# Kernel optimization log

Hardware: AMD Instinct MI355X
Metric: run time of the kernel (lower is better)

## Reference

```python
import math
import jax, jax.numpy as jnp
import numpy as np

I_DIM = 64
N_MODES = 16
FACTOR = 4
EPS = 1e-5


def group_norm(x, w, b):
    # x: [B, M, N, C] channels-last; torch GroupNorm(C//16, C) over (group_channels, M, N)
    B, M, N, C = x.shape
    g = C // 16
    xr = x.reshape(B, M, N, g, C // g)
    mean = xr.mean(axis=(1, 2, 4), keepdims=True)
    var = xr.var(axis=(1, 2, 4), keepdims=True)
    xr = (xr - mean) * jax.lax.rsqrt(var + EPS)
    return xr.reshape(B, M, N, C) * w + b


def feed_forward(x, res, l1w, l1b, l2w, l2b, g1w, g1b, g2w, g2b, g3w, g3b):
    h = x @ l1w + l1b                      # [B,M,N,C*factor]
    h = group_norm(h, g1w, g1b)            # fork_1
    h = jax.nn.relu(h)
    h = h @ l2w + l2b                      # [B,M,N,C]
    h = group_norm(h, g2w, g2b)            # fork_2
    h = res + h
    h = group_norm(h, g3w, g3b)            # fork_3
    return h


def setup_inputs() -> dict:
    key = jax.random.key(0)
    ks = jax.random.split(key, 20)
    B, M, N, I = 4, 128, 128, I_DIM
    H = I * FACTOR
    z = jax.random.normal(ks[0], (B, 2 * M * N * I, 1), dtype=jnp.float32)
    x = jax.random.normal(ks[1], (B, M * N * I, 1), dtype=jnp.float32)
    # fourier weights [in, out, nm, nm, 2], xavier-ish scale
    fw_scale = math.sqrt(2.0 / (I + I))
    fw1 = jax.random.normal(ks[2], (I, I, N_MODES, N_MODES, 2), dtype=jnp.float32) * fw_scale
    fw2 = jax.random.normal(ks[3], (I, I, N_MODES, N_MODES, 2), dtype=jnp.float32) * fw_scale
    def ff_params(k0):
        kk = jax.random.split(k0, 4)
        return dict(
            l1w=jax.random.normal(kk[0], (I, H), dtype=jnp.float32) * math.sqrt(2.0 / (I + H)),
            l1b=jnp.zeros((H,), jnp.float32),
            l2w=jax.random.normal(kk[1], (H, I), dtype=jnp.float32) * math.sqrt(2.0 / (I + H)),
            l2b=jnp.zeros((I,), jnp.float32),
            g1w=jnp.ones((H,), jnp.float32), g1b=jnp.zeros((H,), jnp.float32),
            g2w=jnp.ones((I,), jnp.float32), g2b=jnp.zeros((I,), jnp.float32),
            g3w=jnp.ones((I,), jnp.float32), g3b=jnp.zeros((I,), jnp.float32),
        )
    bp = ff_params(ks[4])
    fp = ff_params(ks[5])
    out = {"z": z, "x": x, "fw1": fw1, "fw2": fw2}
    for name, p in (("b", bp), ("f", fp)):
        for k, v in p.items():
            out[f"{name}_{k}"] = v
    return out


def reference(z, x, fw1, fw2,
              b_l1w, b_l1b, b_l2w, b_l2b, b_g1w, b_g1b, b_g2w, b_g2b, b_g3w, b_g3b,
              f_l1w, f_l1b, f_l2w, f_l2b, f_g1w, f_g1b, f_g2w, f_g2b, f_g3w, f_g3b):
    I = I_DIM
    nm = N_MODES
    B = x.shape[0]
    M = N = int(math.sqrt(x.shape[1] // I))
    x4 = x.reshape(B, M, N, I)
    z5 = z.reshape(B, 2, M, N, I)
    backcast, forecast = z5[:, 0], z5[:, 1]
    x4 = x4 - backcast
    xc = jnp.transpose(x4, (0, 3, 1, 2))          # [B, I, M, N]
    x_ft = jnp.fft.rfft2(xc, s=(M, N), norm='ortho')  # [B, I, M, N//2+1] complex64
    w1 = fw1[..., 0] + 1j * fw1[..., 1]
    w2 = fw2[..., 0] + 1j * fw2[..., 1]
    top = jnp.einsum('bixy,ioxy->boxy', x_ft[:, :, :nm, :nm], w1)
    bot = jnp.einsum('bixy,ioxy->boxy', x_ft[:, :, -nm:, :nm], w2)
    out_ft = jnp.zeros((B, I, N, M // 2 + 1), dtype=x_ft.dtype)
    out_ft = out_ft.at[:, :, :nm, :nm].set(top).at[:, :, -nm:, :nm].set(bot)
    xo = jnp.fft.irfft2(out_ft, s=(N, M), norm='ortho')  # [B, I, M, N]
    xo = jnp.transpose(xo, (0, 2, 3, 1))                  # [B, M, N, I]
    backcast = feed_forward(xo, backcast, b_l1w, b_l1b, b_l2w, b_l2b,
                            b_g1w, b_g1b, b_g2w, b_g2b, b_g3w, b_g3b)
    forecast = feed_forward(xo, forecast, f_l1w, f_l1b, f_l2w, f_l2b,
                            f_g1w, f_g1b, f_g2w, f_g2b, f_g3w, f_g3b)
    out = jnp.stack([backcast, forecast], axis=1)         # [B, 2, M, N, I]
    return out.reshape(B, 2 * M * N * I, 1)
```

## Files before the change

kernel.cpp:

```cpp
#include <hip/hip_runtime.h>
#include <hip/hip_bf16.h>

typedef __hip_bfloat16 bf16;
typedef __attribute__((ext_vector_type(8))) short short8;
typedef __attribute__((ext_vector_type(4))) float f32x4;

#define PI2 6.283185307179586f
#define EPSV 1e-5f

__device__ __forceinline__ short f2bs(float f){
  bf16 h = __float2bfloat16(f);
  short s; __builtin_memcpy(&s, &h, 2); return s;
}
__device__ __forceinline__ float s2f(short s){
  bf16 h; __builtin_memcpy(&h, &s, 2); return __bfloat162float(h);
}
__device__ __forceinline__ float4 f4add(float4 a, float4 b){ return make_float4(a.x+b.x, a.y+b.y, a.z+b.z, a.w+b.w); }
__device__ __forceinline__ float4 f4sub(float4 a, float4 b){ return make_float4(a.x-b.x, a.y-b.y, a.z-b.z, a.w-b.w); }

__global__ __launch_bounds__(256) void k_prep_ydft(
    const float* __restrict__ x, const float* __restrict__ z,
    const float* __restrict__ fw1, const float* __restrict__ fw2,
    float2* __restrict__ FWT,
    const float* __restrict__ b_l1w, const float* __restrict__ b_l1b,
    const float* __restrict__ b_l2w, const float* __restrict__ b_l2b,
    const float* __restrict__ b_g1w, const float* __restrict__ b_g1b,
    const float* __restrict__ b_g2w, const float* __restrict__ b_g2b,
    const float* __restrict__ b_g3w, const float* __restrict__ b_g3b,
    const float* __restrict__ f_l1w, const float* __restrict__ f_l1b,
    const float* __restrict__ f_l2w, const float* __restrict__ f_l2b,
    const float* __restrict__ f_g1w, const float* __restrict__ f_g1b,
    const float* __restrict__ f_g2w, const float* __restrict__ f_g2b,
    const float* __restrict__ f_g3w, const float* __restrict__ f_g3b,
    short* __restrict__ W1g, short* __restrict__ W2g,
    float2* __restrict__ TWY, float2* __restrict__ TWX,
    float* __restrict__ PB, float* __restrict__ ST,
    float2* __restrict__ Y){
  __shared__ __align__(16) char sm[36864];
  int tid = threadIdx.x;
  int bi = blockIdx.x;
  if(bi < 512){
    float2 (*PQ)[64] = (float2(*)[64])sm;
    float2 (*RS)[64] = (float2(*)[64])(sm + 16384);
    float4 (*twl)[32] = (float4(*)[32])(sm + 32768);
    int b = bi >> 7, m = bi & 127;
    const float4* xp = (const float4*)(x + ((size_t)(b*128 + m)*128)*64);
    const float4* zp = (const float4*)(z + ((size_t)((b*2 + 0)*128 + m)*128)*64);
    int i4 = tid & 15, n0 = tid >> 4;
    #pragma unroll
    for(int it = 0; it < 2; it++){
      int np = n0 + it*16;
      float4 ea = f4sub(xp[np*16 + i4],      zp[np*16 + i4]);
      float4 eb = f4sub(xp[(np+32)*16 + i4], zp[(np+32)*16 + i4]);
      float4 ec = f4sub(xp[(np+64)*16 + i4], zp[(np+64)*16 + i4]);
      float4 ed = f4sub(xp[(np+96)*16 + i4], zp[(np+96)*16 + i4]);
      float4 sac = f4add(ea, ec), sbd = f4add(eb, ed);
      float4 P = f4add(sac, sbd), Q = f4sub(sac, sbd);
      float4 R = f4sub(ea, ec),  S = f4sub(eb, ed);
      *(float4*)&PQ[np][i4*4]     = make_float4(P.x, Q.x, P.y, Q.y);
      *(float4*)&PQ[np][i4*4 + 2] = make_float4(P.z, Q.z, P.w, Q.w);
      *(float4*)&RS[np][i4*4]     = make_float4(R.x, S.x, R.y, S.y);
      *(float4*)&RS[np][i4*4 + 2] = make_float4(R.z, S.z, R.w, S.w);
    }
    {
      int kq2 = tid >> 5, np = tid & 31;
      int ky0 = (kq2 >> 1)*4 + (kq2 & 1)*2;
      float s0, c0, s1, c1;
      sincosf(PI2*(float)((ky0*np) & 127)/128.f, &s0, &c0);
      sincosf(PI2*(float)(((ky0+1)*np) & 127)/128.f, &s1, &c1);
      twl[kq2][np] = make_float4(c0, s0, c1, s1);
    }
    __syncthreads();
    int i = tid & 63, kq = tid >> 6;
    float re[4] = {0,0,0,0}, im[4] = {0,0,0,0};
    for(int np = 0; np < 32; np++){
      float2 pq = PQ[np][i];
      float2 rs = RS[np][i];
      float4 t01 = twl[kq*2][np];
      float4 t23 = twl[kq*2 + 1][np];
      re[0] += pq.x*t01.x;               im[0] -= pq.x*t01.y;
      re[1] += rs.x*t01.z - rs.y*t01.w;  im[1] -= rs.y*t01.z + rs.x*t01.w;
      re[2] += pq.y*t23.x;               im[2] -= pq.y*t23.y;
      re[3] += rs.x*t23.z + rs.y*t23.w;  im[3] += rs.y*t23.z - rs.x*t23.w;
    }
    #pragma unroll
    for(int j = 0; j < 4; j++)
      Y[((b*128 + m)*16 + kq*4 + j)*64 + i] = make_float2(re[j], im[j]);
    return;
  }
  if(bi < 1024){
    float (*Ls)[512] = (float(*)[512])sm;
    int bb = bi - 512;
    int arr = bb >> 8, rem = bb & 255;
    int i = rem >> 2, o0 = (rem & 3) * 16;
    const float* src = (arr ? fw2 : fw1) + ((size_t)(i*64 + o0))*512;
    for(int idx = tid; idx < 8192; idx += 256)
      Ls[idx >> 9][idx & 511] = src[idx];
    __syncthreads();
    int kxw = tid >> 4, ky = tid & 15;
    float2* dst = FWT + ((size_t)((arr*16 + kxw)*16 + ky))*4096 + i*64 + o0;
    for(int ol = 0; ol < 16; ol++)
      dst[ol] = make_float2(Ls[ol][tid*2], Ls[ol][tid*2 + 1]);
    return;
  }
  int i = (bi - 1024)*256 + tid;
  if(i < 32768){
    int br = i >> 14, r = i & 16383;
    int fid = r >> 9, lane = (r >> 3) & 63, e = r & 7;
    int hb = fid & 1, t = (fid >> 1) & 3, ch = fid >> 3;
    int l15 = lane & 15, quad = lane >> 4;
    int n = ch*64 + t*16 + l15;
    int k = hb*32 + quad*8 + e;
    const float* src = br ? f_l1w : b_l1w;
    W1g[i] = f2bs(src[k*256 + n]);
    return;
  }
  i -= 32768;
  if(i < 32768){
    int br = i >> 14, r = i & 16383;
    int fid = r >> 9, lane = (r >> 3) & 63, e = r & 7;
    int hb = fid & 1, t = (fid >> 1) & 3, ch = fid >> 3;
    int l15 = lane & 15, quad = lane >> 4;
    int n = t*16 + l15;
    int k = ch*64 + hb*32 + quad*8 + e;
    const float* src = br ? f_l2w : b_l2w;
    W2g[i] = f2bs(src[k*64 + n]);
    return;
  }
  i -= 32768;
  if(i < 2048){
    int ky = i >> 7, n = i & 127;
    float ang = PI2 * (float)((ky*n) & 127) / 128.0f;
    float s, c; sincosf(ang, &s, &c);
    TWY[i] = make_float2(c, s);
    return;
  }
  i -= 2048;
  if(i < 4096){
    int kp = i >> 7, m = i & 127;
    int kx = kp < 16 ? kp : 96 + kp;
    float ang = PI2 * (float)((kx*m) & 127) / 128.0f;
    float s, c; sincosf(ang, &s, &c);
    TWX[i] = make_float2(c, s);
    return;
  }
  i -= 4096;
  if(i < 384){ ST[i] = 0.f; return; }
  i -= 384;
  if(i < 2176){
    int br = i >= 1088; int o = i - br*1088;
    float* pb = PB + br*2048;
    float v;
    if(o < 256)       v = (br ? f_l1b : b_l1b)[o];
    else if(o < 512)  v = (br ? f_g1w : b_g1w)[o-256];
    else if(o < 768)  v = (br ? f_g1b : b_g1b)[o-512];
    else if(o < 832)  v = (br ? f_l2b : b_l2b)[o-768];
    else if(o < 896)  v = (br ? f_g2w : b_g2w)[o-832];
    else if(o < 960)  v = (br ? f_g2b : b_g2b)[o-896];
    else if(o < 1024) v = (br ? f_g3w : b_g3w)[o-960];
    else              v = (br ? f_g3b : b_g3b)[o-1024];
    pb[o] = v;
  }
}

__global__ __launch_bounds__(512) void k_xdft(const float2* __restrict__ Y,
                                              const float2* __restrict__ TWX,
                                              float2* __restrict__ X2){
  __shared__ float2 twl[16][64];
  __shared__ float sc[3][128][8];
  int bi = blockIdx.x;
  int b = bi >> 6, ky = (bi >> 2) & 15, half = (bi >> 1) & 1, ih = bi & 1;
  int tid = threadIdx.x;
  for(int idx = tid; idx < 1024; idx += 512)
    twl[idx >> 6][idx & 63] = TWX[(half*16 + (idx >> 6))*128 + (idx & 63)];
  __syncthreads();
  int i = ih*32 + (tid & 31), grp = (tid >> 5) & 3, mq = tid >> 7;
  const float2* yb = Y + (size_t)b*131072 + ky*64 + i;
  float re[4] = {0,0,0,0}, im[4] = {0,0,0,0};
  for(int mi = 0; mi < 16; mi++){
    int mp = mq*16 + mi;
    float2 y1 = yb[(size_t)mp*1024];
    float2 y2 = yb[(size_t)(mp + 64)*1024];
    float2 ye = make_float2(y1.x + y2.x, y1.y + y2.y);
    float2 yo = make_float2(y1.x - y2.x, y1.y - y2.y);
    float2 t0 = twl[grp*4 + 0][mp];
    float2 t1 = twl[grp*4 + 1][mp];
    float2 t2 = twl[grp*4 + 2][mp];
    float2 t3 = twl[grp*4 + 3][mp];
    re[0] += ye.x*t0.x + ye.y*t0.y;  im[0] += ye.y*t0.x - ye.x*t0.y;
    re[1] += yo.x*t1.x + yo.y*t1.y;  im[1] += yo.y*t1.x - yo.x*t1.y;
    re[2] += ye.x*t2.x + ye.y*t2.y;  im[2] += ye.y*t2.x - ye.x*t2.y;
    re[3] += yo.x*t3.x + yo.y*t3.y;  im[3] += yo.y*t3.x - yo.x*t3.y;
  }
  if(mq){
    int sl = tid & 127;
    #pragma unroll
    for(int j = 0; j < 4; j++){ sc[mq-1][sl][j] = re[j]; sc[mq-1][sl][4 + j] = im[j]; }
  }
  __syncthreads();
  if(!mq){
    const float scn = 1.0f/128.0f;
    #pragma unroll
    for(int j = 0; j < 4; j++){
      float rr = (re[j] + sc[0][tid][j] + sc[1][tid][j] + sc[2][tid][j])*scn;
      float ii = (im[j] + sc[0][tid][4+j] + sc[1][tid][4+j] + sc[2][tid][4+j])*scn;
      int kp = half*16 + grp*4 + j;
      X2[((b*32 + kp)*16 + ky)*64 + i] = make_float2(rr, ii);
    }
  }
}

__global__ __launch_bounds__(512) void k_mix(float2* __restrict__ X2,
                                             const float2* __restrict__ FWT){
  __shared__ float2 Xs[2][4][64];
  __shared__ float sc[3][2][64][8];
  int tid = threadIdx.x;
  {
    int pl = tid >> 8, bq = (tid >> 6) & 3, ii = tid & 63;
    int p = blockIdx.x*2 + pl; int kp = p >> 4, kyy = p & 15;
    Xs[pl][bq][ii] = X2[((bq*32 + kp)*16 + kyy)*64 + ii];
  }
  __syncthreads();
  int o = tid & 63, w = tid >> 6, pl = w >> 2, iq = w & 3;
  int p = blockIdx.x*2 + pl; int kp = p >> 4, ky = p & 15;
  int arr = kp < 16 ? 0 : 1, kxw = kp < 16 ? kp : kp - 16;
  const float2* wp = FWT + ((size_t)((arr*16 + kxw)*16 + ky))*4096;
  float rr[4] = {0,0,0,0}, ii[4] = {0,0,0,0};
  for(int i = iq*16; i < iq*16 + 16; i++){
    float2 wv = wp[i*64 + o];
    #pragma unroll
    for(int b = 0; b < 4; b++){
      float xr = Xs[pl][b][i].x, xi = Xs[pl][b][i].y;
      rr[b] += xr*wv.x - xi*wv.y;
      ii[b] += xr*wv.y + xi*wv.x;
    }
  }
  if(iq){
    #pragma unroll
    for(int b = 0; b < 4; b++){ sc[iq-1][pl][o][b*2] = rr[b]; sc[iq-1][pl][o][b*2 + 1] = ii[b]; }
  }
  __syncthreads();
  if(!iq){
    #pragma unroll
    for(int b = 0; b < 4; b++){
      float r2 = rr[b] + sc[0][pl][o][b*2] + sc[1][pl][o][b*2] + sc[2][pl][o][b*2];
      float i2 = ii[b] + sc[0][pl][o][b*2+1] + sc[1][pl][o][b*2+1] + sc[2][pl][o][b*2+1];
      X2[((b*32 + kp)*16 + ky)*64 + o] = make_float2(r2, i2);
    }
  }
}

__global__ __launch_bounds__(512) void k_inv1(const float2* __restrict__ OF,
                                              const float2* __restrict__ TWX,
                                              float2* __restrict__ T){
  __shared__ float2 Fl[32][16];
  __shared__ float2 twl[32][64];
  __shared__ float sc[256][16];
  int bi = blockIdx.x;
  int b = bi >> 6, ky = (bi >> 2) & 15, oq = bi & 3;
  int tid = threadIdx.x;
  {
    int kp = tid >> 4, ol = tid & 15;
    Fl[kp][ol] = OF[((b*32 + kp)*16 + ky)*64 + oq*16 + ol];
  }
  for(int idx = tid; idx < 2048; idx += 512){
    int kp = idx >> 6, ml = idx & 63;
    twl[kp][ml] = TWX[kp*128 + ml];
  }
  __syncthreads();
  int ol = tid & 15, mg = (tid >> 4) & 15, kh = tid >> 8;
  float reE[4] = {0,0,0,0}, imE[4] = {0,0,0,0};
  float reO[4] = {0,0,0,0}, imO[4] = {0,0,0,0};
  for(int ip = 0; ip < 8; ip++){
    int kp = kh*16 + ip*2;
    float2 fe = Fl[kp][ol], fo = Fl[kp + 1][ol];
    #pragma unroll
    for(int u = 0; u < 4; u++){
      float2 te = twl[kp][mg*4 + u], to = twl[kp + 1][mg*4 + u];
      reE[u] += fe.x*te.x - fe.y*te.y;
      imE[u] += fe.x*te.y + fe.y*te.x;
      reO[u] += fo.x*to.x - fo.y*to.y;
      imO[u] += fo.x*to.y + fo.y*to.x;
    }
  }
  if(kh){
    int sl = tid & 255;
    #pragma unroll
    for(int u = 0; u < 4; u++){
      sc[sl][u] = reE[u]; sc[sl][4 + u] = imE[u];
      sc[sl][8 + u] = reO[u]; sc[sl][12 + u] = imO[u];
    }
  }
  __syncthreads();
  if(!kh){
    int o = oq*16 + ol;
    #pragma unroll
    for(int u = 0; u < 4; u++){
      float rE = reE[u] + sc[tid][u],     iE = imE[u] + sc[tid][4 + u];
      float rO = reO[u] + sc[tid][8 + u], iO = imO[u] + sc[tid][12 + u];
      int ml = mg*4 + u;
      T[((b*128 + ml)*16 + ky)*64 + o]      = make_float2(rE + rO, iE + iO);
      T[((b*128 + ml + 64)*16 + ky)*64 + o] = make_float2(rE - rO, iE - iO);
    }
  }
}

__global__ __launch_bounds__(256) void k_inv2(const float2* __restrict__ T,
                                              const float2* __restrict__ TWY,
                                              bf16* __restrict__ XO,
                                              float* __restrict__ CZ){
  __shared__ float2 twl[16][64];
  int bi = blockIdx.x;
  int b = bi >> 7, m = bi & 127;
  int tid = threadIdx.x;
  int flat = bi*256 + tid;
  if(flat < 16640) CZ[flat] = 0.f;
  for(int idx = tid; idx < 1024; idx += 256)
    twl[idx >> 6][idx & 63] = TWY[(idx >> 6)*128 + (idx & 63)];
  int o = tid & 63, ng = tid >> 6;
  const float2* tp = T + ((size_t)(b*128 + m)*16)*64 + o;
  float t0a = tp[0].x;
  float ax[15], ay[15];
  #pragma unroll
  for(int u = 0; u < 15; u++){
    float2 v = tp[(u + 1)*64];
    ax[u] = 2.f*v.x; ay[u] = 2.f*v.y;
  }
  __syncthreads();
  const float scn = 1.0f/128.0f;
  bf16* xo = XO + ((size_t)(b*128 + m)*128)*64 + o;
  for(int np = ng*16; np < ng*16 + 16; np++){
    float A = t0a, B = 0.f;
    #pragma unroll
    for(int u = 0; u < 15; u++){
      float2 t = twl[u + 1][np];
      float pr = ax[u]*t.x - ay[u]*t.y;
      if(u & 1) A += pr; else B += pr;
    }
    xo[(size_t)np*64]        = __float2bfloat16((A + B)*scn);
    xo[(size_t)(np + 64)*64] = __float2bfloat16((A - B)*scn);
  }
}

__global__ __launch_bounds__(256) void k_cov(const bf16* __restrict__ XO,
                                             float* __restrict__ Cg,
                                             float* __restrict__ SX){
  __shared__ short XT[64][264];
  __shared__ float sxl[64];
  int tid = threadIdx.x;
  int b = blockIdx.x >> 5, ck = blockIdx.x & 31;
  if(tid < 64) sxl[tid] = 0.f;
  float sxp[8];
  #pragma unroll
  for(int e = 0; e < 8; e++) sxp[e] = 0.f;
  int c0 = (tid & 7)*8;
  int lane = tid & 63, w = tid >> 6, l15 = lane & 15, quad = lane >> 4;
  f32x4 acc[4];
  #pragma unroll
  for(int tj = 0; tj < 4; tj++) acc[tj] = (f32x4){0.f,0.f,0.f,0.f};
  for(int st = 0; st < 2; st++){
    size_t pbase = (size_t)b*16384 + (size_t)ck*512 + st*256;
    const short* xg = (const short*)XO + pbase*64;
    __syncthreads();
    for(int it = 0; it < 8; it++){
      int p = it*32 + (tid >> 3);
      short8 v = *(const short8*)(xg + (size_t)p*64 + c0);
      #pragma unroll
      for(int e = 0; e < 8; e++){
        XT[c0+e][p] = v[e];
        sxp[e] += s2f(v[e]);
      }
    }
    __syncthreads();
    for(int kk = 0; kk < 8; kk++){
      short8 a = *(const short8*)&XT[w*16 + l15][kk*32 + quad*8];
      #pragma unroll
      for(int tj = 0; tj < 4; tj++){
        short8 bfr = *(const short8*)&XT[tj*16 + l15][kk*32 + quad*8];
        acc[tj] = __builtin_amdgcn_mfma_f32_16x16x32_bf16(a, bfr, acc[tj], 0, 0, 0);
      }
    }
  }
  #pragma unroll
  for(int e = 0; e < 8; e++) atomicAdd(&sxl[c0+e], sxp[e]);
  __syncthreads();
  float* Cb = Cg + b*4096;
  #pragma unroll
  for(int tj = 0; tj < 4; tj++)
    #pragma unroll
    for(int r = 0; r < 4; r++)
      atomicAdd(&Cb[(w*16 + quad*4 + r)*64 + tj*16 + l15], acc[tj][r]);
  if(tid < 64) atomicAdd(&SX[b*64 + tid], sxl[tid]);
}

__global__ __launch_bounds__(256) void k_stat(const float* __restrict__ Cg,
                                              const float* __restrict__ SX,
                                              const short* __restrict__ W1g,
                                              const float* __restrict__ PB,
                                              float* __restrict__ ST){
  __shared__ float Cl[64][65];
  __shared__ float Wl[16][64];
  __shared__ float sxl[64];
  __shared__ float g2[2];
  int tid = threadIdx.x;
  int br = blockIdx.x >> 6, b = (blockIdx.x >> 4) & 3, g = blockIdx.x & 15;
  const float* Cb = Cg + b*4096;
  for(int u = tid; u < 4096; u += 256) Cl[u >> 6][u & 63] = Cb[u];
  const short* W1 = W1g + br*16384;
  for(int u = tid; u < 1024; u += 256){
    int nl = u >> 6, k = u & 63;
    int n = g*16 + nl;
    int fid = ((n >> 6)*4 + ((n >> 4) & 3))*2 + (k >> 5);
    int lane = ((k >> 3) & 3)*16 + (n & 15);
    Wl[nl][k] = s2f(W1[fid*512 + lane*8 + (k & 7)]);
  }
  if(tid < 64) sxl[tid] = SX[b*64 + tid];
  if(tid < 2) g2[tid] = 0.f;
  __syncthreads();
  int nl = tid >> 4, ic = tid & 15;
  float qa = 0.f, sa = 0.f;
  for(int io = 0; io < 4; io++){
    int i = ic*4 + io;
    float wi = Wl[nl][i];
    float dot = 0.f;
    #pragma unroll 8
    for(int j = 0; j < 64; j++) dot += Cl[i][j]*Wl[nl][j];
    qa += wi*dot;
    sa += wi*sxl[i];
  }
  for(int off = 8; off; off >>= 1){
    qa += __shfl_xor(qa, off);
    sa += __shfl_xor(sa, off);
  }
  if(ic == 0){
    float bn = PB[br*2048 + g*16 + nl];
    float hs = sa + 16384.f*bn;
    float hq = qa + 2.f*bn*sa + 16384.f*bn*bn;
    atomicAdd(&g2[0], hs); atomicAdd(&g2[1], hq);
  }
  __syncthreads();
  if(tid == 0){
    float* S1 = ST + br*192;
    S1[(b*16 + g)*2]     = g2[0];
    S1[(b*16 + g)*2 + 1] = g2[1];
  }
}

__global__ __launch_bounds__(256, 2) void k_ffmain(const bf16* __restrict__ XO,
                                                   const short* __restrict__ W1g,
                                                   const short* __restrict__ W2g,
                                                   const float* __restrict__ PB,
                                                   const float* __restrict__ ST,
                                                   const float* __restrict__ z,
                                                   float* __restrict__ CS,
                                                   float* __restrict__ out){
  __shared__ short Ws1[16384];
  __shared__ short Ws2[16384];
  __shared__ short Hn[64][72];
  __shared__ float mu1[16], rs1[16];
  __shared__ float cs[5][64];
  int tid = threadIdx.x;
  int br = blockIdx.x >> 8, rb = blockIdx.x & 255;
  int r0 = rb << 8, b = rb >> 6;
  const float* pb = PB + br*2048;
  int lane = tid & 63, w = tid >> 6, l15 = lane & 15, quad = lane >> 4;
  int myrow = w*16 + l15;
  short8 a0r[4], a1r[4];
  #pragma unroll
  for(int c = 0; c < 4; c++){
    const short* xop = (const short*)XO + ((size_t)(r0 + c*64 + myrow))*64;
    a0r[c] = *(const short8*)(xop + quad*8);
    a1r[c] = *(const short8*)(xop + 32 + quad*8);
  }
  {
    const uint4* g1 = (const uint4*)(W1g + br*16384);
    const uint4* g2w = (const uint4*)(W2g + br*16384);
    uint4* s1 = (uint4*)Ws1; uint4* s2 = (uint4*)Ws2;
    #pragma unroll
    for(int u = 0; u < 8; u++){
      s1[u*256 + tid] = g1[u*256 + tid];
      s2[u*256 + tid] = g2w[u*256 + tid];
    }
  }
  if(tid < 16){
    const float cnt = 262144.f;
    const float* S1 = ST + br*192;
    float s = S1[(b*16 + tid)*2], q = S1[(b*16 + tid)*2 + 1];
    float mean = s/cnt, var = q/cnt - mean*mean;
    mu1[tid] = mean; rs1[tid] = rsqrtf(fmaxf(var, 0.f) + EPSV);
  }
  {
    float* c1 = &cs[0][0];
    c1[tid] = 0.f;
    if(tid < 64) c1[256 + tid] = 0.f;
  }
  __syncthreads();
  float sh[4]  = {0,0,0,0}, sh2[4] = {0,0,0,0};
  float sz[4]  = {0,0,0,0}, sz2[4] = {0,0,0,0}, shz[4] = {0,0,0,0};
  #pragma unroll
  for(int c = 0; c < 4; c++){
    size_t obase_off = ((size_t)(b*2 + br)*16384 + (r0 & 16383) + c*64)*64;
    const float* zbase = z + obase_off;
    float zr[16];
    #pragma unroll
    for(int t = 0; t < 4; t++)
      #pragma unroll
      for(int r = 0; r < 4; r++)
        zr[t*4 + r] = zbase[(size_t)(w*16 + quad*4 + r)*64 + t*16 + l15];
    f32x4 acc2[4];
    #pragma unroll
    for(int t = 0; t < 4; t++) acc2[t] = (f32x4){0.f,0.f,0.f,0.f};
    for(int ch = 0; ch < 4; ch++){
      #pragma unroll
      for(int t = 0; t < 4; t++){
        int fid = (ch*4 + t)*2;
        short8 b0 = *(const short8*)(Ws1 + fid*512 + lane*8);
        short8 b1 = *(const short8*)(Ws1 + fid*512 + 512 + lane*8);
        f32x4 acc = {0.f,0.f,0.f,0.f};
        acc = __builtin_amdgcn_mfma_f32_16x16x32_bf16(a0r[c], b0, acc, 0, 0, 0);
        acc = __builtin_amdgcn_mfma_f32_16x16x32_bf16(a1r[c], b1, acc, 0, 0, 0);
        int n = ch*64 + t*16 + l15, gi = n >> 4;
        float w1v = pb[256 + n];
        float gwv = w1v * rs1[gi];
        float gbv = (pb[n] - mu1[gi])*rs1[gi]*w1v + pb[512 + n];
        #pragma unroll
        for(int r = 0; r < 4; r++){
          float hv = acc[r]*gwv + gbv;
          hv = hv > 0.f ? hv : 0.f;
          Hn[w*16 + quad*4 + r][t*16 + l15] = f2bs(hv);
        }
      }
      short8 ha0 = *(short8*)&Hn[myrow][quad*8];
      short8 ha1 = *(short8*)&Hn[myrow][32 + quad*8];
      #pragma unroll
      for(int t = 0; t < 4; t++){
        int fid = (ch*4 + t)*2;
        short8 b0 = *(const short8*)(Ws2 + fid*512 + lane*8);
        short8 b1 = *(const short8*)(Ws2 + fid*512 + 512 + lane*8);
        acc2[t] = __builtin_amdgcn_mfma_f32_16x16x32_bf16(ha0, b0, acc2[t], 0, 0, 0);
        acc2[t] = __builtin_amdgcn_mfma_f32_16x16x32_bf16(ha1, b1, acc2[t], 0, 0, 0);
      }
    }
    float* obase = out + obase_off;
    #pragma unroll
    for(int t = 0; t < 4; t++){
      int col = t*16 + l15;
      float bias2 = pb[768 + col];
      #pragma unroll
      for(int r = 0; r < 4; r++){
        size_t off = (size_t)(w*16 + quad*4 + r)*64 + col;
        float h2 = acc2[t][r] + bias2;
        float zv = zr[t*4 + r];
        obase[off] = h2;
        sh[t] += h2; sh2[t] += h2*h2;
        sz[t] += zv; sz2[t] += zv*zv; shz[t] += h2*zv;
      }
    }
  }
  #pragma unroll
  for(int t = 0; t < 4; t++){
    float v0 = sh[t], v1 = sh2[t], v2 = sz[t], v3 = sz2[t], v4 = shz[t];
    v0 += __shfl_xor(v0, 16); v0 += __shfl_xor(v0, 32);
    v1 += __shfl_xor(v1, 16); v1 += __shfl_xor(v1, 32);
    v2 += __shfl_xor(v2, 16); v2 += __shfl_xor(v2, 32);
    v3 += __shfl_xor(v3, 16); v3 += __shfl_xor(v3, 32);
    v4 += __shfl_xor(v4, 16); v4 += __shfl_xor(v4, 32);
    if(quad == 0){
      int ch = t*16 + l15;
      atomicAdd(&cs[0][ch], v0); atomicAdd(&cs[1][ch], v1);
      atomicAdd(&cs[2][ch], v2); atomicAdd(&cs[3][ch], v3);
      atomicAdd(&cs[4][ch], v4);
    }
  }
  __syncthreads();
  float* slab = CS + (size_t)blockIdx.x*320;
  const float* c1 = &cs[0][0];
  slab[tid] = c1[tid];
  if(tid < 64) slab[256 + tid] = c1[256 + tid];
}

__global__ __launch_bounds__(256) void k_statB(const float* __restrict__ CS,
                                               const float* __restrict__ PB,
                                               float* __restrict__ CF){
  __shared__ float chs[5][64];
  __shared__ float mu2s[4], rs2s[4], tg[4], tq[4], mu3s[4], rs3s[4];
  int br = blockIdx.x >> 2, b = blockIdx.x & 3;
  int tid = threadIdx.x;
  const float* base = CS + ((size_t)(br*256 + b*64))*320;
  float* c1 = &chs[0][0];
  for(int v = tid; v < 320; v += 256){
    float s = 0.f;
    for(int k = 0; k < 64; k++) s += base[(size_t)k*320 + v];
    c1[v] = s;
  }
  __syncthreads();
  if(tid < 4){
    float s = 0.f, q = 0.f;
    for(int o = tid*16; o < tid*16 + 16; o++){ s += chs[0][o]; q += chs[1][o]; }
    float mean = s/262144.f, var = q/262144.f - mean*mean;
    mu2s[tid] = mean; rs2s[tid] = rsqrtf(fmaxf(var, 0.f) + EPSV);
    tg[tid] = 0.f; tq[tid] = 0.f;
  }
  __syncthreads();
  const float* pb = PB + br*2048;
  if(tid < 64){
    int o = tid, g = o >> 4;
    float w2v = pb[832 + o], b2v = pb[896 + o];
    float gw = w2v*rs2s[g], gb = b2v - mu2s[g]*rs2s[g]*w2v;
    float Sh = chs[0][o], Sh2 = chs[1][o], Sz = chs[2][o], Sz2 = chs[3][o], Shz = chs[4][o];
    float st = gw*Sh + Sz + 16384.f*gb;
    float sq = gw*gw*Sh2 + Sz2 + 16384.f*gb*gb + 2.f*gw*Shz + 2.f*gw*gb*Sh + 2.f*gb*Sz;
    atomicAdd(&tg[g], st); atomicAdd(&tq[g], sq);
  }
  __syncthreads();
  if(tid < 4){
    float mean = tg[tid]/262144.f, var = tq[tid]/262144.f - mean*mean;
    mu3s[tid] = mean; rs3s[tid] = rsqrtf(fmaxf(var, 0.f) + EPSV);
  }
  __syncthreads();
  if(tid < 64){
    int o = tid, g = o >> 4;
    float w2v = pb[832 + o], b2v = pb[896 + o];
    float gw = w2v*rs2s[g], gb = b2v - mu2s[g]*rs2s[g]*w2v;
    float w3v = pb[960 + o], b3v = pb[1024 + o];
    float gw3 = w3v*rs3s[g], gb3 = b3v - mu3s[g]*rs3s[g]*w3v;
    float* cf = CF + (size_t)(br*4 + b)*192;
    cf[o]       = gw*gw3;
    cf[64 + o]  = gw3;
    cf[128 + o] = gb*gw3 + gb3;
  }
}

__global__ __launch_bounds__(256) void k_final(const float* __restrict__ z,
                                               const float* __restrict__ CF,
                                               float* __restrict__ out){
  int tid = blockIdx.x*256 + threadIdx.x;
  const float4* z4 = (const float4*)z;
  const float4* cf4 = (const float4*)CF;
  float4* o4 = (float4*)out;
  #pragma unroll
  for(int r = 0; r < 8; r++){
    int i4 = r*262144 + tid;
    int s = i4 >> 18;
    int b = s >> 1, br = s & 1;
    int cbase = (br*4 + b)*48 + (i4 & 15);
    float4 a = cf4[cbase], bb = cf4[cbase + 16], g = cf4[cbase + 32];
    float4 h = o4[i4], zv = z4[i4];
    o4[i4] = make_float4(h.x*a.x + zv.x*bb.x + g.x,
                         h.y*a.y + zv.y*bb.y + g.y,
                         h.z*a.z + zv.z*bb.z + g.z,
                         h.w*a.w + zv.w*bb.w + g.w);
  }
}

extern "C" void kernel_launch(void* const* d_in, const int* in_sizes, int n_in,
                              void* d_out, int out_size, void* d_ws, size_t ws_size,
                              hipStream_t stream){
  const float* z   = (const float*)d_in[0];
  const float* x   = (const float*)d_in[1];
  const float* fw1 = (const float*)d_in[2];
  const float* fw2 = (const float*)d_in[3];
  char* ws = (char*)d_ws;
  float2* Y   = (float2*)(ws + 0);
  float2* X2  = (float2*)(ws + 4194304);
  float2* T   = Y;
  bf16*   XO  = (bf16*)(ws + 5242880);
  float*  ST  = (float*)(ws + 13631488);
  short*  W1g = (short*)(ws + 13633536);
  short*  W2g = (short*)(ws + 13699072);
  float2* TWY = (float2*)(ws + 13764608);
  float2* TWX = (float2*)(ws + 13780992);
  float*  PB  = (float*)(ws + 13813760);
  float2* FWT = (float2*)(ws + 13830144);
  float*  Cg  = (float*)(ws + 13830144);
  float*  SX  = Cg + 16384;
  float*  CS  = (float*)(ws + 14878720);
  float*  CF  = (float*)(ws + 15927296);

  const float* p[20];
  for(int i = 0; i < 20; i++) p[i] = (const float*)d_in[4 + i];

  k_prep_ydft<<<1314, 256, 0, stream>>>(x, z, fw1, fw2, FWT,
                                  p[0],p[1],p[2],p[3],p[4],p[5],p[6],p[7],p[8],p[9],
                                  p[10],p[11],p[12],p[13],p[14],p[15],p[16],p[17],p[18],p[19],
                                  W1g, W2g, TWY, TWX, PB, ST, Y);
  k_xdft<<<256, 512, 0, stream>>>(Y, TWX, X2);
  k_mix<<<256, 512, 0, stream>>>(X2, FWT);
  k_inv1<<<256, 512, 0, stream>>>(X2, TWX, T);
  k_inv2<<<512, 256, 0, stream>>>(T, TWY, XO, Cg);
  k_cov<<<128, 256, 0, stream>>>(XO, Cg, SX);
  k_stat<<<128, 256, 0, stream>>>(Cg, SX, W1g, PB, ST);
  k_ffmain<<<512, 256, 0, stream>>>(XO, W1g, W2g, PB, ST, z, CS, (float*)d_out);
  k_statB<<<8, 256, 0, stream>>>(CS, PB, CF);
  k_final<<<1024, 256, 0, stream>>>(z, CF, (float*)d_out);
}
```

Baseline: 247.3 us.

## Compute spatial covariance from spectral coefficients via Parseval, merge with inverse DFT

The channel covariance and channel sums needed for the first group norm are now computed directly from the truncated Fourier coefficients (Parseval), in extra blocks of the first inverse-DFT kernel. This replaces the old covariance kernel, which reread the whole spatial bf16 activation. The Y intermediate is re-laid out so that x-DFT loads are contiguous. The FF output is staged as bf16 instead of fp32 before the final affine pass, which halves that traffic but lowers precision.

```diff
diff --git a/kernel.cpp b/kernel.cpp
--- a/kernel.cpp
+++ b/kernel.cpp
@@ -85,7 +85,7 @@
     }
     #pragma unroll
     for(int j = 0; j < 4; j++)
-      Y[((b*128 + m)*16 + kq*4 + j)*64 + i] = make_float2(re[j], im[j]);
+      Y[(((size_t)b*16 + kq*4 + j)*128 + m)*64 + i] = make_float2(re[j], im[j]);
     return;
   }
   if(bi < 1024){
@@ -165,22 +165,25 @@
 
 __global__ __launch_bounds__(512) void k_xdft(const float2* __restrict__ Y,
                                               const float2* __restrict__ TWX,
-                                              float2* __restrict__ X2){
+                                              float2* __restrict__ X2,
+                                              float* __restrict__ CgZ){
   __shared__ float2 twl[16][64];
   __shared__ float sc[3][128][8];
   int bi = blockIdx.x;
   int b = bi >> 6, ky = (bi >> 2) & 15, half = (bi >> 1) & 1, ih = bi & 1;
   int tid = threadIdx.x;
+  int flat = bi*512 + tid;
+  if(flat < 16384) CgZ[flat] = 0.f;
   for(int idx = tid; idx < 1024; idx += 512)
     twl[idx >> 6][idx & 63] = TWX[(half*16 + (idx >> 6))*128 + (idx & 63)];
   __syncthreads();
   int i = ih*32 + (tid & 31), grp = (tid >> 5) & 3, mq = tid >> 7;
-  const float2* yb = Y + (size_t)b*131072 + ky*64 + i;
+  const float2* yb = Y + ((size_t)(b*16 + ky)*128)*64 + i;
   float re[4] = {0,0,0,0}, im[4] = {0,0,0,0};
   for(int mi = 0; mi < 16; mi++){
     int mp = mq*16 + mi;
-    float2 y1 = yb[(size_t)mp*1024];
-    float2 y2 = yb[(size_t)(mp + 64)*1024];
+    float2 y1 = yb[(size_t)mp*64];
+    float2 y2 = yb[(size_t)(mp + 64)*64];
     float2 ye = make_float2(y1.x + y2.x, y1.y + y2.y);
     float2 yo = make_float2(y1.x - y2.x, y1.y - y2.y);
     float2 t0 = twl[grp*4 + 0][mp];
@@ -250,147 +253,123 @@
   }
 }
 
-__global__ __launch_bounds__(512) void k_inv1(const float2* __restrict__ OF,
-                                              const float2* __restrict__ TWX,
-                                              float2* __restrict__ T){
-  __shared__ float2 Fl[32][16];
-  __shared__ float2 twl[32][64];
-  __shared__ float sc[256][16];
+__global__ __launch_bounds__(512) void k_inv1scov(const float2* __restrict__ OF,
+                                                  const float2* __restrict__ TWX,
+                                                  float* __restrict__ Cg,
+                                                  float* __restrict__ SX,
+                                                  float2* __restrict__ T){
+  __shared__ __align__(16) char smu[36864];
   int bi = blockIdx.x;
-  int b = bi >> 6, ky = (bi >> 2) & 15, oq = bi & 3;
   int tid = threadIdx.x;
+  if(bi < 256){
+    float2 (*Fl)[16]  = (float2(*)[16])smu;
+    float2 (*twl)[64] = (float2(*)[64])(smu + 4096);
+    float  (*sc)[16]  = (float(*)[16])(smu + 20480);
+    int b = bi >> 6, ky = (bi >> 2) & 15, oq = bi & 3;
+    {
+      int kp = tid >> 4, ol = tid & 15;
+      Fl[kp][ol] = OF[((b*32 + kp)*16 + ky)*64 + oq*16 + ol];
+    }
+    for(int idx = tid; idx < 2048; idx += 512){
+      int kp = idx >> 6, ml = idx & 63;
+      twl[kp][ml] = TWX[kp*128 + ml];
+    }
+    __syncthreads();
+    int ol = tid & 15, mg = (tid >> 4) & 15, kh = tid >> 8;
+    float reE[4] = {0,0,0,0}, imE[4] = {0,0,0,0};
+    float reO[4] = {0,0,0,0}, imO[4] = {0,0,0,0};
+    for(int ip = 0; ip < 8; ip++){
+      int kp = kh*16 + ip*2;
+      float2 fe = Fl[kp][ol], fo = Fl[kp + 1][ol];
+      #pragma unroll
+      for(int u = 0; u < 4; u++){
+        float2 te = twl[kp][mg*4 + u], to = twl[kp + 1][mg*4 + u];
+        reE[u] += fe.x*te.x - fe.y*te.y;
+        imE[u] += fe.x*te.y + fe.y*te.x;
+        reO[u] += fo.x*to.x - fo.y*to.y;
+        imO[u] += fo.x*to.y + fo.y*to.x;
+      }
+    }
+    if(kh){
+      int sl = tid & 255;
+      #pragma unroll
+      for(int u = 0; u < 4; u++){
+        sc[sl][u] = reE[u]; sc[sl][4 + u] = imE[u];
+        sc[sl][8 + u] = reO[u]; sc[sl][12 + u] = imO[u];
+      }
+    }
+    __syncthreads();
+    if(!kh){
+      int o = oq*16 + ol;
+      #pragma unroll
+      for(int u = 0; u < 4; u++){
+        float rE = reE[u] + sc[tid][u],     iE = imE[u] + sc[tid][4 + u];
+        float rO = reO[u] + sc[tid][8 + u], iO = imO[u] + sc[tid][12 + u];
+        int ml = mg*4 + u;
+        T[((b*128 + ml)*16 + ky)*64 + o]      = make_float2(rE + rO, iE + iO);
+        T[((b*128 + ml + 64)*16 + ky)*64 + o] = make_float2(rE - rO, iE - iO);
+      }
+    }
+    return;
+  }
   {
-    int kp = tid >> 4, ol = tid & 15;
-    Fl[kp][ol] = OF[((b*32 + kp)*16 + ky)*64 + oq*16 + ol];
-  }
-  for(int idx = tid; idx < 2048; idx += 512){
-    int kp = idx >> 6, ml = idx & 63;
-    twl[kp][ml] = TWX[kp*128 + ml];
-  }
-  __syncthreads();
-  int ol = tid & 15, mg = (tid >> 4) & 15, kh = tid >> 8;
-  float reE[4] = {0,0,0,0}, imE[4] = {0,0,0,0};
-  float reO[4] = {0,0,0,0}, imO[4] = {0,0,0,0};
-  for(int ip = 0; ip < 8; ip++){
-    int kp = kh*16 + ip*2;
-    float2 fe = Fl[kp][ol], fo = Fl[kp + 1][ol];
-    #pragma unroll
-    for(int u = 0; u < 4; u++){
-      float2 te = twl[kp][mg*4 + u], to = twl[kp + 1][mg*4 + u];
-      reE[u] += fe.x*te.x - fe.y*te.y;
-      imE[u] += fe.x*te.y + fe.y*te.x;
-      reO[u] += fo.x*to.x - fo.y*to.y;
-      imO[u] += fo.x*to.y + fo.y*to.x;
-    }
-  }
-  if(kh){
-    int sl = tid & 255;
-    #pragma unroll
-    for(int u = 0; u < 4; u++){
-      sc[sl][u] = reE[u]; sc[sl][4 + u] = imE[u];
-      sc[sl][8 + u] = reO[u]; sc[sl][12 + u] = imO[u];
-    }
-  }
-  __syncthreads();
-  if(!kh){
-    int o = oq*16 + ol;
-    #pragma unroll
-    for(int u = 0; u < 4; u++){
-      float rE = reE[u] + sc[tid][u],     iE = imE[u] + sc[tid][4 + u];
-      float rO = reO[u] + sc[tid][8 + u], iO = imO[u] + sc[tid][12 + u];
-      int ml = mg*4 + u;
-      T[((b*128 + ml)*16 + ky)*64 + o]      = make_float2(rE + rO, iE + iO);
-      T[((b*128 + ml + 64)*16 + ky)*64 + o] = make_float2(rE - rO, iE - iO);
-    }
-  }
-}
-
-__global__ __launch_bounds__(256) void k_inv2(const float2* __restrict__ T,
-                                              const float2* __restrict__ TWY,
-                                              bf16* __restrict__ XO,
-                                              float* __restrict__ CZ){
-  __shared__ float2 twl[16][64];
-  int bi = blockIdx.x;
-  int b = bi >> 7, m = bi & 127;
-  int tid = threadIdx.x;
-  int flat = bi*256 + tid;
-  if(flat < 16640) CZ[flat] = 0.f;
-  for(int idx = tid; idx < 1024; idx += 256)
-    twl[idx >> 6][idx & 63] = TWY[(idx >> 6)*128 + (idx & 63)];
-  int o = tid & 63, ng = tid >> 6;
-  const float2* tp = T + ((size_t)(b*128 + m)*16)*64 + o;
-  float t0a = tp[0].x;
-  float ax[15], ay[15];
-  #pragma unroll
-  for(int u = 0; u < 15; u++){
-    float2 v = tp[(u + 1)*64];
-    ax[u] = 2.f*v.x; ay[u] = 2.f*v.y;
-  }
-  __syncthreads();
-  const float scn = 1.0f/128.0f;
-  bf16* xo = XO + ((size_t)(b*128 + m)*128)*64 + o;
-  for(int np = ng*16; np < ng*16 + 16; np++){
-    float A = t0a, B = 0.f;
-    #pragma unroll
-    for(int u = 0; u < 15; u++){
-      float2 t = twl[u + 1][np];
-      float pr = ax[u]*t.x - ay[u]*t.y;
-      if(u & 1) A += pr; else B += pr;
-    }
-    xo[(size_t)np*64]        = __float2bfloat16((A + B)*scn);
-    xo[(size_t)(np + 64)*64] = __float2bfloat16((A - B)*scn);
-  }
-}
-
-__global__ __launch_bounds__(256) void k_cov(const bf16* __restrict__ XO,
-                                             float* __restrict__ Cg,
-                                             float* __restrict__ SX){
-  __shared__ short XT[64][264];
-  __shared__ float sxl[64];
-  int tid = threadIdx.x;
-  int b = blockIdx.x >> 5, ck = blockIdx.x & 31;
-  if(tid < 64) sxl[tid] = 0.f;
-  float sxp[8];
-  #pragma unroll
-  for(int e = 0; e < 8; e++) sxp[e] = 0.f;
-  int c0 = (tid & 7)*8;
-  int lane = tid & 63, w = tid >> 6, l15 = lane & 15, quad = lane >> 4;
-  f32x4 acc[4];
-  #pragma unroll
-  for(int tj = 0; tj < 4; tj++) acc[tj] = (f32x4){0.f,0.f,0.f,0.f};
-  for(int st = 0; st < 2; st++){
-    size_t pbase = (size_t)b*16384 + (size_t)ck*512 + st*256;
-    const short* xg = (const short*)XO + pbase*64;
+    short (*XT)[264] = (short(*)[264])smu;
+    int sb = bi - 256;
+    int b = sb >> 2, q = sb & 3;
+    const float RT2 = 1.41421356237f, RTH = 0.70710678118f;
+    int c0 = (tid & 7)*8;
+    #pragma unroll
+    for(int it = 0; it < 4; it++){
+      int pl = it*64 + (tid >> 3);
+      int rg = q*256 + pl;
+      int bin = rg >> 1, reim = rg & 1;
+      int kp = bin >> 4, ky = bin & 15;
+      const float2* base = OF + ((size_t)((b*32 + kp)*16 + ky))*64;
+      #pragma unroll
+      for(int e = 0; e < 8; e++){
+        int i = c0 + e;
+        float v;
+        if(ky){
+          float2 t = base[i];
+          v = (reim ? t.y : t.x)*RT2;
+        } else if(kp == 0){
+          v = reim ? 0.f : base[i].x;
+        } else if(kp < 16){
+          const float2* mb = OF + ((size_t)((b*32 + (32 - kp))*16))*64;
+          float2 t = base[i], u2 = mb[i];
+          v = (reim ? 0.5f*(t.y - u2.y) : 0.5f*(t.x + u2.x))*RT2;
+        } else if(kp == 16){
+          float2 t = base[i];
+          v = (reim ? t.y : t.x)*RTH;
+        } else {
+          v = 0.f;
+        }
+        XT[i][pl] = f2bs(v);
+      }
+    }
+    if(q == 0 && tid < 64)
+      SX[b*64 + tid] = 128.f * OF[((size_t)(b*32)*16)*64 + tid].x;
     __syncthreads();
-    for(int it = 0; it < 8; it++){
-      int p = it*32 + (tid >> 3);
-      short8 v = *(const short8*)(xg + (size_t)p*64 + c0);
-      #pragma unroll
-      for(int e = 0; e < 8; e++){
-        XT[c0+e][p] = v[e];
-        sxp[e] += s2f(v[e]);
-      }
-    }
-    __syncthreads();
-    for(int kk = 0; kk < 8; kk++){
-      short8 a = *(const short8*)&XT[w*16 + l15][kk*32 + quad*8];
+    int lane = tid & 63, w8 = tid >> 6, wr = w8 & 3, kh = w8 >> 2;
+    int l15 = lane & 15, quad = lane >> 4;
+    f32x4 acc[4];
+    #pragma unroll
+    for(int tj = 0; tj < 4; tj++) acc[tj] = (f32x4){0.f,0.f,0.f,0.f};
+    for(int kk = kh*4; kk < kh*4 + 4; kk++){
+      short8 a = *(const short8*)&XT[wr*16 + l15][kk*32 + quad*8];
       #pragma unroll
       for(int tj = 0; tj < 4; tj++){
         short8 bfr = *(const short8*)&XT[tj*16 + l15][kk*32 + quad*8];
         acc[tj] = __builtin_amdgcn_mfma_f32_16x16x32_bf16(a, bfr, acc[tj], 0, 0, 0);
       }
     }
-  }
-  #pragma unroll
-  for(int e = 0; e < 8; e++) atomicAdd(&sxl[c0+e], sxp[e]);
-  __syncthreads();
-  float* Cb = Cg + b*4096;
-  #pragma unroll
-  for(int tj = 0; tj < 4; tj++)
-    #pragma unroll
-    for(int r = 0; r < 4; r++)
-      atomicAdd(&Cb[(w*16 + quad*4 + r)*64 + tj*16 + l15], acc[tj][r]);
-  if(tid < 64) atomicAdd(&SX[b*64 + tid], sxl[tid]);
+    float* Cb = Cg + b*4096;
+    #pragma unroll
+    for(int tj = 0; tj < 4; tj++)
+      #pragma unroll
+      for(int r = 0; r < 4; r++)
+        atomicAdd(&Cb[(wr*16 + quad*4 + r)*64 + tj*16 + l15], acc[tj][r]);
+  }
 }
 
 __global__ __launch_bounds__(256) void k_stat(const float* __restrict__ Cg,
@@ -446,6 +425,40 @@
   }
 }
 
+__global__ __launch_bounds__(256) void k_inv2(const float2* __restrict__ T,
+                                              const float2* __restrict__ TWY,
+                                              bf16* __restrict__ XO){
+  __shared__ float2 twl[16][64];
+  int bi = blockIdx.x;
+  int b = bi >> 7, m = bi & 127;
+  int tid = threadIdx.x;
+  for(int idx = tid; idx < 1024; idx += 256)
+    twl[idx >> 6][idx & 63] = TWY[(idx >> 6)*128 + (idx & 63)];
+  int o = tid & 63, ng = tid >> 6;
+  const float2* tp = T + ((size_t)(b*128 + m)*16)*64 + o;
+  float t0a = tp[0].x;
+  float ax[15], ay[15];
+  #pragma unroll
+  for(int u = 0; u < 15; u++){
+    float2 v = tp[(u + 1)*64];
+    ax[u] = 2.f*v.x; ay[u] = 2.f*v.y;
+  }
+  __syncthreads();
+  const float scn = 1.0f/128.0f;
+  bf16* xo = XO + ((size_t)(b*128 + m)*128)*64 + o;
+  for(int np = ng*16; np < ng*16 + 16; np++){
+    float A = t0a, B = 0.f;
+    #pragma unroll
+    for(int u = 0; u < 15; u++){
+      float2 t = twl[u + 1][np];
+      float pr = ax[u]*t.x - ay[u]*t.y;
+      if(u & 1) A += pr; else B += pr;
+    }
+    xo[(size_t)np*64]        = __float2bfloat16((A + B)*scn);
+    xo[(size_t)(np + 64)*64] = __float2bfloat16((A - B)*scn);
+  }
+}
+
 __global__ __launch_bounds__(256, 2) void k_ffmain(const bf16* __restrict__ XO,
                                                    const short* __restrict__ W1g,
                                                    const short* __restrict__ W2g,
@@ -453,7 +466,7 @@
                                                    const float* __restrict__ ST,
                                                    const float* __restrict__ z,
                                                    float* __restrict__ CS,
-                                                   float* __restrict__ out){
+                                                   unsigned short* __restrict__ H2){
   __shared__ short Ws1[16384];
   __shared__ short Ws2[16384];
   __shared__ short Hn[64][72];
@@ -541,7 +554,7 @@
         acc2[t] = __builtin_amdgcn_mfma_f32_16x16x32_bf16(ha1, b1, acc2[t], 0, 0, 0);
       }
     }
-    float* obase = out + obase_off;
+    unsigned short* hbase = H2 + obase_off;
     #pragma unroll
     for(int t = 0; t < 4; t++){
       int col = t*16 + l15;
@@ -551,7 +564,7 @@
         size_t off = (size_t)(w*16 + quad*4 + r)*64 + col;
         float h2 = acc2[t][r] + bias2;
         float zv = zr[t*4 + r];
-        obase[off] = h2;
+        hbase[off] = (unsigned short)f2bs(h2);
         sh[t] += h2; sh2[t] += h2*h2;
         sz[t] += zv; sz2[t] += zv*zv; shz[t] += h2*zv;
       }
@@ -633,10 +646,12 @@
 
 __global__ __launch_bounds__(256) void k_final(const float* __restrict__ z,
                                                const float* __restrict__ CF,
+                                               const unsigned short* __restrict__ H2,
                                                float* __restrict__ out){
   int tid = blockIdx.x*256 + threadIdx.x;
   const float4* z4 = (const float4*)z;
   const float4* cf4 = (const float4*)CF;
+  const ushort4* h4 = (const ushort4*)H2;
   float4* o4 = (float4*)out;
   #pragma unroll
   for(int r = 0; r < 8; r++){
@@ -645,11 +660,12 @@
     int b = s >> 1, br = s & 1;
     int cbase = (br*4 + b)*48 + (i4 & 15);
     float4 a = cf4[cbase], bb = cf4[cbase + 16], g = cf4[cbase + 32];
-    float4 h = o4[i4], zv = z4[i4];
-    o4[i4] = make_float4(h.x*a.x + zv.x*bb.x + g.x,
-                         h.y*a.y + zv.y*bb.y + g.y,
-                         h.z*a.z + zv.z*bb.z + g.z,
-                         h.w*a.w + zv.w*bb.w + g.w);
+    ushort4 hu = h4[i4];
+    float4 zv = z4[i4];
+    o4[i4] = make_float4(s2f((short)hu.x)*a.x + zv.x*bb.x + g.x,
+                         s2f((short)hu.y)*a.y + zv.y*bb.y + g.y,
+                         s2f((short)hu.z)*a.z + zv.z*bb.z + g.z,
+                         s2f((short)hu.w)*a.w + zv.w*bb.w + g.w);
   }
 }
 
@@ -672,10 +688,11 @@
   float2* TWX = (float2*)(ws + 13780992);
   float*  PB  = (float*)(ws + 13813760);
   float2* FWT = (float2*)(ws + 13830144);
-  float*  Cg  = (float*)(ws + 13830144);
-  float*  SX  = Cg + 16384;
   float*  CS  = (float*)(ws + 14878720);
   float*  CF  = (float*)(ws + 15927296);
+  unsigned short* H2 = (unsigned short*)(ws + 16777216);
+  float*  Cg  = (float*)(ws + 33554432);
+  float*  SX  = Cg + 16384;
 
   const float* p[20];
   for(int i = 0; i < 20; i++) p[i] = (const float*)d_in[4 + i];
@@ -684,13 +701,12 @@
                                   p[0],p[1],p[2],p[3],p[4],p[5],p[6],p[7],p[8],p[9],
                                   p[10],p[11],p[12],p[13],p[14],p[15],p[16],p[17],p[18],p[19],
                                   W1g, W2g, TWY, TWX, PB, ST, Y);
-  k_xdft<<<256, 512, 0, stream>>>(Y, TWX, X2);
+  k_xdft<<<256, 512, 0, stream>>>(Y, TWX, X2, Cg);
   k_mix<<<256, 512, 0, stream>>>(X2, FWT);
-  k_inv1<<<256, 512, 0, stream>>>(X2, TWX, T);
-  k_inv2<<<512, 256, 0, stream>>>(T, TWY, XO, Cg);
-  k_cov<<<128, 256, 0, stream>>>(XO, Cg, SX);
+  k_inv1scov<<<272, 512, 0, stream>>>(X2, TWX, Cg, SX, T);
   k_stat<<<128, 256, 0, stream>>>(Cg, SX, W1g, PB, ST);
-  k_ffmain<<<512, 256, 0, stream>>>(XO, W1g, W2g, PB, ST, z, CS, (float*)d_out);
+  k_inv2<<<512, 256, 0, stream>>>(T, TWY, XO);
+  k_ffmain<<<512, 256, 0, stream>>>(XO, W1g, W2g, PB, ST, z, CS, H2);
   k_statB<<<8, 256, 0, stream>>>(CS, PB, CF);
-  k_final<<<1024, 256, 0, stream>>>(z, CF, (float*)d_out);
-}
+  k_final<<<1024, 256, 0, stream>>>(z, CF, H2, (float*)d_out);
+}
```

After: 240.5 us. 1.03x faster.
